# Optimization experiments

Measured on AMD Instinct MI355X. Metric: run time of the kernel, lower is better.

## Reference

```python
import jax, jax.numpy as jnp
import numpy as np

N_NODES = 100000
DEG = 16
N_EDGES = N_NODES * DEG
D_IN = 64
D_OUT = 64


def setup_inputs() -> dict:
    key = jax.random.key(0)
    k1, k2, k3 = jax.random.split(key, 3)
    X = jax.random.normal(k1, (N_NODES, D_IN), dtype=jnp.float32)
    stdv = 1.0 / np.sqrt(D_OUT)
    weight = jax.random.uniform(k2, (D_IN, D_OUT), dtype=jnp.float32, minval=-stdv, maxval=stdv)
    # CSR: fixed out-degree DEG per node (regularized for reproducible setup)
    row_pointers = (jnp.arange(N_NODES + 1, dtype=jnp.int64) * DEG)
    column_index = jax.random.randint(k3, (N_EDGES,), 0, N_NODES, dtype=jnp.int32)
    # GCN normalization: degrees[i] = 1/sqrt(d_i)
    counts = (row_pointers[1:] - row_pointers[:-1]).astype(jnp.float32)
    degrees = 1.0 / jnp.sqrt(jnp.maximum(counts, 1.0))
    return {"X": X, "weight": weight, "row_pointers": row_pointers,
            "column_index": column_index, "degrees": degrees}


def reference(X, weight, row_pointers, column_index, degrees):
    # Feature transform first (D_OUT <= D_IN keeps aggregation traffic low)
    xw = X @ weight                                   # [N, D_OUT]
    counts = row_pointers[1:] - row_pointers[:-1]     # [N]
    dst = jnp.repeat(jnp.arange(N_NODES, dtype=jnp.int32), counts,
                     total_repeat_length=N_EDGES)     # [E] destination node per edge
    src = column_index                                # [E] neighbor (source) per edge
    norm = degrees[dst] * degrees[src]                # [E] d_i^{-1/2} d_j^{-1/2}
    msgs = xw[src] * norm[:, None]                    # [E, D_OUT]
    out = jax.ops.segment_sum(msgs, dst, num_segments=N_NODES)  # [N, D_OUT]
    return out
```

## Files before the change

### kernel.cpp

```cpp
#include <hip/hip_runtime.h>

#define D 64

static __device__ __forceinline__ unsigned int bf16r(float f) {
    const unsigned int u = __float_as_uint(f);
    return (u + 0x7fffu + ((u >> 16) & 1u)) >> 16;
}

__global__ __launch_bounds__(256, 2)
void gcn_xw_tile(const float* __restrict__ X, const float* __restrict__ W,
                 const float* __restrict__ deg, ushort* __restrict__ Y,
                 int n_nodes)
{
    __shared__ float Xs[64][132];
    __shared__ float Ws[64][64];

    const int t  = threadIdx.x;
    const int m0 = blockIdx.x * 128;

    {
        const float4* __restrict__ W4 = (const float4*)W;
        float4* Ws4 = (float4*)&Ws[0][0];
#pragma unroll
        for (int r = 0; r < 4; ++r) Ws4[t + 256 * r] = W4[t + 256 * r];
    }

#pragma unroll
    for (int r = 0; r < 8; ++r) {
        const int q   = t + 256 * r;
        const int m   = q >> 4;
        const int kg  = q & 15;
        const int row = m0 + m;
        float4 xv = make_float4(0.f, 0.f, 0.f, 0.f);
        if (row < n_nodes) xv = ((const float4*)(X + (size_t)row * D))[kg];
        Xs[4 * kg + 0][m] = xv.x;
        Xs[4 * kg + 1][m] = xv.y;
        Xs[4 * kg + 2][m] = xv.z;
        Xs[4 * kg + 3][m] = xv.w;
    }
    __syncthreads();

    const int tx = t & 15;
    const int ty = t >> 4;

    float acc[8][4];
#pragma unroll
    for (int i = 0; i < 8; ++i)
#pragma unroll
        for (int j = 0; j < 4; ++j) acc[i][j] = 0.f;

#pragma unroll 8
    for (int k = 0; k < 64; ++k) {
        const float4 wv = *(const float4*)&Ws[k][4 * tx];
        const float4 xa = *(const float4*)&Xs[k][8 * ty];
        const float4 xb = *(const float4*)&Xs[k][8 * ty + 4];
#define ROWFMA(i, xs)                                   \
        acc[i][0] = fmaf(xs, wv.x, acc[i][0]);          \
        acc[i][1] = fmaf(xs, wv.y, acc[i][1]);          \
        acc[i][2] = fmaf(xs, wv.z, acc[i][2]);          \
        acc[i][3] = fmaf(xs, wv.w, acc[i][3]);
        ROWFMA(0, xa.x) ROWFMA(1, xa.y) ROWFMA(2, xa.z) ROWFMA(3, xa.w)
        ROWFMA(4, xb.x) ROWFMA(5, xb.y) ROWFMA(6, xb.z) ROWFMA(7, xb.w)
#undef ROWFMA
    }

#pragma unroll
    for (int i = 0; i < 8; ++i) {
        const int node = m0 + 8 * ty + i;
        if (node < n_nodes) {
            const float dn = deg[node];
            uint2 v;
            v.x = bf16r(acc[i][0] * dn) | (bf16r(acc[i][1] * dn) << 16);
            v.y = bf16r(acc[i][2] * dn) | (bf16r(acc[i][3] * dn) << 16);
            *(uint2*)(Y + (size_t)node * D + 4 * tx) = v;
        }
    }
}

__global__ __launch_bounds__(256, 4)
void gcn_gather4(const ushort* __restrict__ Y, const int* __restrict__ rp,
                 const int* __restrict__ col, const float* __restrict__ deg,
                 float* __restrict__ out, int n_nodes)
{
    const int lane   = threadIdx.x & 63;
    const int s      = lane >> 4;
    const int f      = lane & 15;
    const int gwave  = (int)((blockIdx.x * blockDim.x + threadIdx.x) >> 6);
    const int nwaves = (int)((gridDim.x * blockDim.x) >> 6);
    const int ngroups = (n_nodes + 3) >> 2;

    for (int g = gwave; g < ngroups; g += nwaves) {
        const int  n     = g * 4 + s;
        const bool valid = (n < n_nodes);
        const int  rpn   = valid ? rp[n]     : 0;
        const int  rpe   = valid ? rp[n + 1] : 0;
        const int  dcnt  = rpe - rpn;

        const bool ok = !valid || (dcnt == 16 && (rpn & 3) == 0);
        if (__ballot(ok) == ~0ull) {
            int idx[16];
            *(int4*)(idx + 0)  = *(const int4*)(col + rpn + 0);
            *(int4*)(idx + 4)  = *(const int4*)(col + rpn + 4);
            *(int4*)(idx + 8)  = *(const int4*)(col + rpn + 8);
            *(int4*)(idx + 12) = *(const int4*)(col + rpn + 12);

            float a0 = 0.f, a1 = 0.f, a2 = 0.f, a3 = 0.f;
#pragma unroll
            for (int j = 0; j < 16; ++j) {
                const uint2 u = *(const uint2*)(Y + ((size_t)idx[j] << 6) + (f << 2));
                a0 += __uint_as_float(u.x << 16);
                a1 += __uint_as_float(u.x & 0xffff0000u);
                a2 += __uint_as_float(u.y << 16);
                a3 += __uint_as_float(u.y & 0xffff0000u);
            }
            if (valid) {
                const float dn = deg[n];
                float4 v;
                v.x = a0 * dn; v.y = a1 * dn; v.z = a2 * dn; v.w = a3 * dn;
                *(float4*)(out + (size_t)n * D + f * 4) = v;
            }
        } else if (valid) {
            float a0 = 0.f, a1 = 0.f, a2 = 0.f, a3 = 0.f;
            for (int e = rpn; e < rpe; ++e) {
                const int sj = col[e];
                const uint2 u = *(const uint2*)(Y + ((size_t)sj << 6) + (f << 2));
                a0 += __uint_as_float(u.x << 16);
                a1 += __uint_as_float(u.x & 0xffff0000u);
                a2 += __uint_as_float(u.y << 16);
                a3 += __uint_as_float(u.y & 0xffff0000u);
            }
            const float dn = deg[n];
            float4 v;
            v.x = a0 * dn; v.y = a1 * dn; v.z = a2 * dn; v.w = a3 * dn;
            *(float4*)(out + (size_t)n * D + f * 4) = v;
        }
    }
}

static __device__ __forceinline__ float bcast_f(float v, int l) {
    return __uint_as_float(__builtin_amdgcn_readlane(__float_as_uint(v), l));
}

__global__ __launch_bounds__(256, 4)
void gcn_fused_kernel(const float* __restrict__ X, const float* __restrict__ W,
                      const int* __restrict__ rp, const int* __restrict__ col,
                      const float* __restrict__ deg, float* __restrict__ out,
                      int n_nodes)
{
    const int lane   = threadIdx.x & 63;
    const int gwave  = (int)((blockIdx.x * blockDim.x + threadIdx.x) >> 6);
    const int nwaves = (int)((gridDim.x * blockDim.x) >> 6);

    for (int node = gwave; node < n_nodes; node += nwaves) {
        const int start = rp[node];
        const int end   = rp[node + 1];
        const float di  = deg[node];
        float h = 0.f;

        for (int e0 = start; e0 < end; e0 += 64) {
            const int cnt = min(64, end - e0);
            int   s_  = (lane < cnt) ? col[e0 + lane] : 0;
            float nm_ = (lane < cnt) ? di * deg[s_] : 0.f;
            for (int j = 0; j < cnt; ++j) {
                const int   sj = __builtin_amdgcn_readlane(s_, j);
                const float nj = bcast_f(nm_, j);
                h = fmaf(nj, X[(size_t)sj * D + lane], h);
            }
        }

        float c0 = 0.f, c1 = 0.f, c2 = 0.f, c3 = 0.f;
#pragma unroll
        for (int l = 0; l < D; l += 4) {
            c0 = fmaf(bcast_f(h, l + 0), W[(l + 0) * D + lane], c0);
            c1 = fmaf(bcast_f(h, l + 1), W[(l + 1) * D + lane], c1);
            c2 = fmaf(bcast_f(h, l + 2), W[(l + 2) * D + lane], c2);
            c3 = fmaf(bcast_f(h, l + 3), W[(l + 3) * D + lane], c3);
        }
        out[(size_t)node * D + lane] = (c0 + c1) + (c2 + c3);
    }
}

extern "C" void kernel_launch(void* const* d_in, const int* in_sizes, int n_in,
                              void* d_out, int out_size, void* d_ws, size_t ws_size,
                              hipStream_t stream) {
    const float* X   = (const float*)d_in[0];
    const float* W   = (const float*)d_in[1];
    const int*   rp  = (const int*)d_in[2];
    const int*   col = (const int*)d_in[3];
    const float* deg = (const float*)d_in[4];
    float* out = (float*)d_out;

    const int n_nodes = in_sizes[4];
    const size_t y_bytes = (size_t)n_nodes * D * sizeof(ushort);

    if (ws_size >= y_bytes) {
        ushort* Y = (ushort*)d_ws;
        const int k1_blocks = (n_nodes + 127) / 128;
        gcn_xw_tile<<<k1_blocks, 256, 0, stream>>>(X, W, deg, Y, n_nodes);
        gcn_gather4<<<2048, 256, 0, stream>>>(Y, rp, col, deg, out, n_nodes);
    } else {
        gcn_fused_kernel<<<1024, 256, 0, stream>>>(X, W, rp, col, deg, out, n_nodes);
    }
}
```

Measured before the change: 130.9 us.

## Make XW transform kernel persistent with register prefetch of next X tile

The dense transform kernel becomes a persistent grid of at most 768 blocks that loop over 128-row tiles. Each block loads W into shared memory once and prefetches the next tile's X rows into registers while it computes the current one. The aim is to amortize the W load and hide global-load latency behind the FMA loop. In exchange it uses more registers (a second prefetch array) and an extra barrier per tile, which could lower occupancy.

```diff
diff --git a/kernel.cpp b/kernel.cpp
--- a/kernel.cpp
+++ b/kernel.cpp
@@ -8,15 +8,16 @@
 }
 
 __global__ __launch_bounds__(256, 2)
-void gcn_xw_tile(const float* __restrict__ X, const float* __restrict__ W,
+void gcn_xw_pipe(const float* __restrict__ X, const float* __restrict__ W,
                  const float* __restrict__ deg, ushort* __restrict__ Y,
-                 int n_nodes)
+                 int n_nodes, int ntiles)
 {
     __shared__ float Xs[64][132];
     __shared__ float Ws[64][64];
 
     const int t  = threadIdx.x;
-    const int m0 = blockIdx.x * 128;
+    const int tx = t & 15;
+    const int ty = t >> 4;
 
     {
         const float4* __restrict__ W4 = (const float4*)W;
@@ -25,55 +26,80 @@
         for (int r = 0; r < 4; ++r) Ws4[t + 256 * r] = W4[t + 256 * r];
     }
 
-#pragma unroll
-    for (int r = 0; r < 8; ++r) {
-        const int q   = t + 256 * r;
-        const int m   = q >> 4;
-        const int kg  = q & 15;
-        const int row = m0 + m;
-        float4 xv = make_float4(0.f, 0.f, 0.f, 0.f);
-        if (row < n_nodes) xv = ((const float4*)(X + (size_t)row * D))[kg];
-        Xs[4 * kg + 0][m] = xv.x;
-        Xs[4 * kg + 1][m] = xv.y;
-        Xs[4 * kg + 2][m] = xv.z;
-        Xs[4 * kg + 3][m] = xv.w;
-    }
-    __syncthreads();
-
-    const int tx = t & 15;
-    const int ty = t >> 4;
-
-    float acc[8][4];
-#pragma unroll
-    for (int i = 0; i < 8; ++i)
-#pragma unroll
-        for (int j = 0; j < 4; ++j) acc[i][j] = 0.f;
+    const float4 f4z = make_float4(0.f, 0.f, 0.f, 0.f);
+    float4 pf[8];
+
+    int tile = blockIdx.x;
+    if (tile < ntiles) {
+        const int m0 = tile * 128;
+#pragma unroll
+        for (int r = 0; r < 8; ++r) {
+            const int row = m0 + ty + 16 * r;
+            pf[r] = (row < n_nodes) ? ((const float4*)(X + (size_t)row * D))[tx]
+                                    : f4z;
+        }
+    }
+
+    for (; tile < ntiles; tile += gridDim.x) {
+#pragma unroll
+        for (int r = 0; r < 8; ++r) {
+            const int m = ty + 16 * r;
+            Xs[4 * tx + 0][m] = pf[r].x;
+            Xs[4 * tx + 1][m] = pf[r].y;
+            Xs[4 * tx + 2][m] = pf[r].z;
+            Xs[4 * tx + 3][m] = pf[r].w;
+        }
+        __syncthreads();
+
+        const int nxt = tile + gridDim.x;
+        float4 pn[8];
+        if (nxt < ntiles) {
+            const int m0n = nxt * 128;
+#pragma unroll
+            for (int r = 0; r < 8; ++r) {
+                const int row = m0n + ty + 16 * r;
+                pn[r] = (row < n_nodes)
+                          ? ((const float4*)(X + (size_t)row * D))[tx] : f4z;
+            }
+        }
+
+        float acc[8][4];
+#pragma unroll
+        for (int i = 0; i < 8; ++i)
+#pragma unroll
+            for (int j = 0; j < 4; ++j) acc[i][j] = 0.f;
 
 #pragma unroll 8
-    for (int k = 0; k < 64; ++k) {
-        const float4 wv = *(const float4*)&Ws[k][4 * tx];
-        const float4 xa = *(const float4*)&Xs[k][8 * ty];
-        const float4 xb = *(const float4*)&Xs[k][8 * ty + 4];
+        for (int k = 0; k < 64; ++k) {
+            const float4 wv = *(const float4*)&Ws[k][4 * tx];
+            const float4 xa = *(const float4*)&Xs[k][8 * ty];
+            const float4 xb = *(const float4*)&Xs[k][8 * ty + 4];
 #define ROWFMA(i, xs)                                   \
-        acc[i][0] = fmaf(xs, wv.x, acc[i][0]);          \
-        acc[i][1] = fmaf(xs, wv.y, acc[i][1]);          \
-        acc[i][2] = fmaf(xs, wv.z, acc[i][2]);          \
-        acc[i][3] = fmaf(xs, wv.w, acc[i][3]);
-        ROWFMA(0, xa.x) ROWFMA(1, xa.y) ROWFMA(2, xa.z) ROWFMA(3, xa.w)
-        ROWFMA(4, xb.x) ROWFMA(5, xb.y) ROWFMA(6, xb.z) ROWFMA(7, xb.w)
+            acc[i][0] = fmaf(xs, wv.x, acc[i][0]);      \
+            acc[i][1] = fmaf(xs, wv.y, acc[i][1]);      \
+            acc[i][2] = fmaf(xs, wv.z, acc[i][2]);      \
+            acc[i][3] = fmaf(xs, wv.w, acc[i][3]);
+            ROWFMA(0, xa.x) ROWFMA(1, xa.y) ROWFMA(2, xa.z) ROWFMA(3, xa.w)
+            ROWFMA(4, xb.x) ROWFMA(5, xb.y) ROWFMA(6, xb.z) ROWFMA(7, xb.w)
 #undef ROWFMA
-    }
-
-#pragma unroll
-    for (int i = 0; i < 8; ++i) {
-        const int node = m0 + 8 * ty + i;
-        if (node < n_nodes) {
-            const float dn = deg[node];
-            uint2 v;
-            v.x = bf16r(acc[i][0] * dn) | (bf16r(acc[i][1] * dn) << 16);
-            v.y = bf16r(acc[i][2] * dn) | (bf16r(acc[i][3] * dn) << 16);
-            *(uint2*)(Y + (size_t)node * D + 4 * tx) = v;
-        }
+        }
+
+        const int m0 = tile * 128;
+#pragma unroll
+        for (int i = 0; i < 8; ++i) {
+            const int node = m0 + 8 * ty + i;
+            if (node < n_nodes) {
+                const float dn = deg[node];
+                uint2 v;
+                v.x = bf16r(acc[i][0] * dn) | (bf16r(acc[i][1] * dn) << 16);
+                v.y = bf16r(acc[i][2] * dn) | (bf16r(acc[i][3] * dn) << 16);
+                *(uint2*)(Y + (size_t)node * D + 4 * tx) = v;
+            }
+        }
+        __syncthreads();
+
+#pragma unroll
+        for (int r = 0; r < 8; ++r) pf[r] = pn[r];
     }
 }
 
@@ -195,8 +221,9 @@
 
     if (ws_size >= y_bytes) {
         ushort* Y = (ushort*)d_ws;
-        const int k1_blocks = (n_nodes + 127) / 128;
-        gcn_xw_tile<<<k1_blocks, 256, 0, stream>>>(X, W, deg, Y, n_nodes);
+        const int ntiles = (n_nodes + 127) / 128;
+        const int k1_blocks = ntiles < 768 ? ntiles : 768;
+        gcn_xw_pipe<<<k1_blocks, 256, 0, stream>>>(X, W, deg, Y, n_nodes, ntiles);
         gcn_gather4<<<2048, 256, 0, stream>>>(Y, rp, col, deg, out, n_nodes);
     } else {
         gcn_fused_kernel<<<1024, 256, 0, stream>>>(X, W, rp, col, deg, out, n_nodes);
```

After: 131.2 us. About the same (+0.3%).
